# Kernel tuning notes

Measured on AMD Instinct MI355X. Metric: run time of the kernel, lower is better.

Reference implementation:

```python
import jax, jax.numpy as jnp
import numpy as np

B, LX, T = 32, 64, 128
D = 512          # d_model
DW = 512         # d_word_vec
V = 32000        # src_vocab_size
AV = 16          # trg_vocab_size (attribute vocab)
YL = 2
LSTM_IN = 2 * DW + 2 * D  # decode_on_y=True


def setup_inputs() -> dict:
    key = jax.random.key(0)
    ks = jax.random.split(key, 20)
    s = 0.02
    attr_tab = jax.random.normal(ks[10], (AV, DW), jnp.float32) * s
    attr_tab = attr_tab.at[0].set(0.0)  # padding_idx=0
    return {
        "x_enc": jax.random.normal(ks[0], (B, LX, 2 * D), jnp.float32),
        "x_enc_k": jax.random.normal(ks[1], (B, LX, D), jnp.float32),
        "dec_h0": jax.random.normal(ks[2], (B, D), jnp.float32),
        "dec_c0": jax.random.normal(ks[3], (B, D), jnp.float32),
        "x_mask": jnp.zeros((B, LX), jnp.bool_),
        "y_train": jax.random.randint(ks[4], (B, YL), 0, AV),
        "x_train": jax.random.randint(ks[5], (B, T), 0, V),
        "word_emb": jax.random.normal(ks[6], (V, DW), jnp.float32) * s,
        "attr_emb_tab": attr_tab,
        "W_ih": jax.random.normal(ks[7], (4 * D, LSTM_IN), jnp.float32) * s,
        "W_hh": jax.random.normal(ks[8], (4 * D, D), jnp.float32) * s,
        "b_ih": jnp.zeros((4 * D,), jnp.float32),
        "b_hh": jnp.zeros((4 * D,), jnp.float32),
        "W_trg": jax.random.normal(ks[9], (D, D), jnp.float32) * s,
        "b_trg": jnp.zeros((D,), jnp.float32),
        "W_att": jax.random.normal(ks[11], (1, D), jnp.float32) * s,
        "b_att": jnp.zeros((1,), jnp.float32),
        "W_cr": jax.random.normal(ks[12], (D, 3 * D), jnp.float32) * s,
        "W_ro": jax.random.normal(ks[13], (V, D), jnp.float32) * s,
    }


def _decode(x_enc, x_enc_k, dec_h0, dec_c0, y_train, x_train, word_emb,
            attr_emb_tab, W_ih, W_hh, b_ih, b_hh, W_trg, b_trg, W_att, b_att,
            W_cr, W_ro):
    x_emb = word_emb[x_train[:, :-1]]          # [B, T-1, DW]
    attr = attr_emb_tab[y_train].sum(axis=1)   # [B, DW]

    def step(carry, x_t):
        h, c, feed = carry
        inp = jnp.concatenate([x_t, attr, feed], axis=1)  # [B, 2DW+2D]
        gates = inp @ W_ih.T + b_ih + h @ W_hh.T + b_hh   # [B, 4D]
        i, f, g, o = jnp.split(gates, 4, axis=1)          # torch order i,f,g,o
        c = jax.nn.sigmoid(f) * c + jax.nn.sigmoid(i) * jnp.tanh(g)
        h = jax.nn.sigmoid(o) * jnp.tanh(c)
        # MlpAttn (attn_mask is ignored in the original)
        q = h @ W_trg.T + b_trg                            # [B, D]
        att_h = jnp.tanh(x_enc_k + q[:, None, :])          # [B, LX, D]
        scores = (att_h @ W_att.T + b_att)[..., 0]         # [B, LX]
        w = jax.nn.softmax(scores, axis=-1)
        ctx = jnp.einsum('bl,bld->bd', w, x_enc)           # [B, 2D]
        pre = jnp.tanh(jnp.concatenate([h, ctx], axis=1) @ W_cr.T)  # [B, D]
        return (h, c, ctx), pre

    feed0 = jnp.zeros((x_enc.shape[0], 2 * D), x_enc.dtype)
    xs = jnp.swapaxes(x_emb, 0, 1)                         # [T-1, B, DW]
    _, pres = jax.lax.scan(step, (dec_h0, dec_c0, feed0), xs)  # [T-1, B, D]
    logits = jnp.einsum('tbd,vd->btv', pres, W_ro)         # [B, T-1, V]
    return logits


def reference(x_enc, x_enc_k, dec_h0, dec_c0, x_mask, y_train, x_train,
              word_emb, attr_emb_tab, W_ih, W_hh, b_ih, b_hh, W_trg, b_trg,
              W_att, b_att, W_cr, W_ro):
    return _decode(x_enc, x_enc_k, dec_h0, dec_c0, y_train, x_train, word_emb,
                   attr_emb_tab, W_ih, W_hh, b_ih, b_hh, W_trg, b_trg, W_att,
                   b_att, W_cr, W_ro)
```

## Files before the change

kernel.cpp:

```cpp
#include <hip/hip_runtime.h>
#include <stdint.h>

typedef unsigned short u16;
using bf16x8 = __attribute__((ext_vector_type(8))) short;
using f32x4  = __attribute__((ext_vector_type(4))) float;

__device__ __forceinline__ float b2f(u16 v) {
  return __uint_as_float(((uint32_t)v) << 16);
}
__device__ __forceinline__ u16 f2b(float f) {
  uint32_t u = __float_as_uint(f);
  u = u + 0x7fffu + ((u >> 16) & 1u);
  return (u16)(u >> 16);
}
__device__ __forceinline__ float ldf(const void* p, size_t i, int f32) {
  return f32 ? ((const float*)p)[i] : b2f(((const u16*)p)[i]);
}
__device__ __forceinline__ float sigf(float x) {
  return __builtin_amdgcn_rcpf(1.f + __expf(-x));
}
__device__ __forceinline__ float tanhf_fast(float x) {
  x = fminf(fmaxf(x, -15.f), 15.f);
  float e = __expf(2.f * x);
  return (e - 1.f) * __builtin_amdgcn_rcpf(e + 1.f);
}

__global__ __launch_bounds__(1024) void k_detect(const u16* __restrict__ x, int* flag) {
  int tid = threadIdx.x;
  u16 v = x[tid];
  int e = (v >> 7) & 0xFF;
  int ok = (e >= 100 && e <= 140) ? 1 : 0;
#pragma unroll
  for (int o = 32; o > 0; o >>= 1) ok += __shfl_down(ok, o);
  __shared__ int s[16];
  if ((tid & 63) == 0) s[tid >> 6] = ok;
  __syncthreads();
  if (tid == 0) {
    int c = 0;
#pragma unroll
    for (int i = 0; i < 16; ++i) c += s[i];
    *flag = (c < 900) ? 1 : 0;
  }
}

__global__ __launch_bounds__(256) void k_conv(u16* __restrict__ dst, const void* __restrict__ src,
                                              int n, const int* __restrict__ flagp) {
  int f32 = *flagp;
  int i = blockIdx.x * 256 + threadIdx.x;
  if (i < n) dst[i] = f32 ? f2b(((const float*)src)[i]) : ((const u16*)src)[i];
}

__global__ __launch_bounds__(256) void k_bias(float* __restrict__ bias, const void* b_ih,
                                              const void* b_hh, const int* __restrict__ flagp) {
  int f32 = *flagp;
  int n = blockIdx.x * 256 + threadIdx.x;
  if (n < 2048) bias[n] = ldf(b_ih, n, f32) + ldf(b_hh, n, f32);
}

template<int EPI>
__global__ __launch_bounds__(256) void gemm_bt(
    const u16* __restrict__ A, int lda,
    const void* __restrict__ B, int ldb,
    int M, int K,
    void* __restrict__ C,
    const float* __restrict__ bias,
    int ldc, const int* __restrict__ flagp)
{
  __shared__ __align__(16) u16 As[128 * 32];
  __shared__ __align__(16) u16 Bs[128 * 32];
  const int f32  = *flagp;
  const int tid  = threadIdx.x;
  const int lane = tid & 63;
  const int wv   = tid >> 6;
  const int wm   = (wv >> 1) * 64;
  const int wn   = (wv & 1) * 64;
  const int n0   = blockIdx.x * 128;
  const int m0   = blockIdx.y * 128;
  const int lr   = lane & 15;
  const int lk   = (lane >> 4) * 8;

  f32x4 acc[4][4] = {};

  for (int k0 = 0; k0 < K; k0 += 32) {
    __syncthreads();
#pragma unroll
    for (int c = 0; c < 2; ++c) {
      int idx = tid + c * 256;
      int row = idx >> 2;
      int col = (idx & 3) * 8;
      int ar = m0 + row; if (ar > M - 1) ar = M - 1;
      *(uint4*)&As[idx * 8] = *(const uint4*)&A[(size_t)ar * lda + k0 + col];
      int br = n0 + row;
      if (f32) {
        const float* bp = (const float*)B + (size_t)br * ldb + k0 + col;
        float4 x0 = *(const float4*)bp;
        float4 x1 = *(const float4*)(bp + 4);
        uint4 pk;
        pk.x = (uint32_t)f2b(x0.x) | ((uint32_t)f2b(x0.y) << 16);
        pk.y = (uint32_t)f2b(x0.z) | ((uint32_t)f2b(x0.w) << 16);
        pk.z = (uint32_t)f2b(x1.x) | ((uint32_t)f2b(x1.y) << 16);
        pk.w = (uint32_t)f2b(x1.z) | ((uint32_t)f2b(x1.w) << 16);
        *(uint4*)&Bs[idx * 8] = pk;
      } else {
        *(uint4*)&Bs[idx * 8] = *(const uint4*)((const u16*)B + (size_t)br * ldb + k0 + col);
      }
    }
    __syncthreads();
    bf16x8 af[4], bfr[4];
#pragma unroll
    for (int i = 0; i < 4; ++i) {
      af[i]  = *(const bf16x8*)&As[(wm + i * 16 + lr) * 32 + lk];
      bfr[i] = *(const bf16x8*)&Bs[(wn + i * 16 + lr) * 32 + lk];
    }
#pragma unroll
    for (int i = 0; i < 4; ++i)
#pragma unroll
      for (int j = 0; j < 4; ++j)
        acc[i][j] = __builtin_amdgcn_mfma_f32_16x16x32_bf16(af[i], bfr[j], acc[i][j], 0, 0, 0);
  }

#pragma unroll
  for (int i = 0; i < 4; ++i) {
#pragma unroll
    for (int j = 0; j < 4; ++j) {
#pragma unroll
      for (int r = 0; r < 4; ++r) {
        int m = m0 + wm + i * 16 + (lane >> 4) * 4 + r;
        int n = n0 + wn + j * 16 + lr;
        if (m < M) {
          float v = acc[i][j][r];
          if (EPI == 0) {
            ((u16*)C)[(size_t)m * ldc + n] = f2b(v + bias[n]);
          } else if (EPI == 1) {
            ((u16*)C)[(size_t)m * ldc + n] = f2b(tanhf_fast(v));
          } else {
            int tt = m >> 5, bb = m & 31;
            size_t off = (size_t)bb * 4064000 + (size_t)tt * 32000 + n;
            if (f32) ((float*)C)[off] = v;
            else     ((u16*)C)[off] = f2b(v);
          }
        }
      }
    }
  }
}

__global__ __launch_bounds__(256) void k_step(
    const u16* __restrict__ inp,
    const u16* __restrict__ W3,
    const u16* __restrict__ pregates_t,
    float* __restrict__ c_state,
    u16* __restrict__ inp_next,
    u16* __restrict__ hctx_t)
{
  const int tid  = threadIdx.x;
  const int lane = tid & 63;
  const int g    = tid >> 6;
  const int c0   = blockIdx.x * 16;
  const int lr   = lane & 15;
  const int lk   = (lane >> 4) * 8;

  f32x4 acc0 = {}, acc1 = {};
  const u16* Ar = inp + lr * 1536 + lk;
  const u16* Br = W3 + (size_t)(g * 512 + c0 + lr) * 1536 + lk;
#pragma unroll 8
  for (int k0 = 0; k0 < 1536; k0 += 32) {
    bf16x8 a0 = *(const bf16x8*)(Ar + k0);
    bf16x8 a1 = *(const bf16x8*)(Ar + 16 * 1536 + k0);
    bf16x8 b  = *(const bf16x8*)(Br + k0);
    acc0 = __builtin_amdgcn_mfma_f32_16x16x32_bf16(a0, b, acc0, 0, 0, 0);
    acc1 = __builtin_amdgcn_mfma_f32_16x16x32_bf16(a1, b, acc1, 0, 0, 0);
  }

  __shared__ float gs[4][32][16];
#pragma unroll
  for (int r = 0; r < 4; ++r) {
    int mr = (lane >> 4) * 4 + r;
    gs[g][mr][lr]      = acc0[r] + b2f(pregates_t[mr * 2048 + g * 512 + c0 + lr]);
    gs[g][mr + 16][lr] = acc1[r] + b2f(pregates_t[(mr + 16) * 2048 + g * 512 + c0 + lr]);
  }
  __syncthreads();

  for (int e = tid; e < 512; e += 256) {
    int m = e >> 4, j = e & 15;
    int col = c0 + j;
    float iv = gs[0][m][j], fv = gs[1][m][j], gv = gs[2][m][j], ov = gs[3][m][j];
    float co = c_state[m * 512 + col];
    float cn = sigf(fv) * co + sigf(iv) * tanhf_fast(gv);
    float h  = sigf(ov) * tanhf_fast(cn);
    c_state[m * 512 + col] = cn;
    u16 hb = f2b(h);
    inp_next[m * 1536 + 1024 + col] = hb;
    hctx_t[m * 1536 + col] = hb;
  }
}

__global__ __launch_bounds__(512) void k_att(
    const u16* __restrict__ inp_next,
    const u16* __restrict__ x_enc_k,
    const u16* __restrict__ x_enc,
    const u16* __restrict__ W_trg,
    const u16* __restrict__ b_trg,
    const u16* __restrict__ W_att,
    const u16* __restrict__ b_att,
    u16* __restrict__ hctx_t,
    u16* __restrict__ feed_dst)
{
  const int b   = blockIdx.x;
  const int tid = threadIdx.x;
  __shared__ float hs[512], qs[512], wa[512], sc[64], wts[64];

  hs[tid] = b2f(inp_next[b * 1536 + 1024 + tid]);
  wa[tid] = b2f(W_att[tid]);
  __syncthreads();

  {
    float q = b2f(b_trg[tid]);
    const u16* wr = W_trg + tid * 512;
#pragma unroll 4
    for (int kk = 0; kk < 64; ++kk) {
      int k = kk * 8;
      bf16x8 w8 = *(const bf16x8*)(wr + k);
#pragma unroll
      for (int j = 0; j < 8; ++j)
        q += b2f((u16)w8[j]) * hs[k + j];
    }
    qs[tid] = q;
  }
  __syncthreads();

  const int wvv = tid >> 6, ln = tid & 63;
  for (int l = wvv; l < 64; l += 8) {
    float p = 0.f;
    const u16* xk = x_enc_k + ((size_t)b * 64 + l) * 512;
#pragma unroll
    for (int dd = 0; dd < 8; ++dd) {
      int d = ln + dd * 64;
      p += wa[d] * tanhf_fast(b2f(xk[d]) + qs[d]);
    }
#pragma unroll
    for (int o = 32; o > 0; o >>= 1) p += __shfl_down(p, o);
    if (ln == 0) sc[l] = p + b2f(b_att[0]);
  }
  __syncthreads();
  if (tid < 64) {
    float s = sc[tid];
    float mx = s;
#pragma unroll
    for (int o = 32; o > 0; o >>= 1) mx = fmaxf(mx, __shfl_xor(mx, o));
    float e = __expf(s - mx);
    float sm = e;
#pragma unroll
    for (int o = 32; o > 0; o >>= 1) sm += __shfl_xor(sm, o);
    wts[tid] = e * __builtin_amdgcn_rcpf(sm);
  }
  __syncthreads();
  {
    int d2 = tid * 2;
    float a0 = 0.f, a1 = 0.f;
    const u16* xe = x_enc + (size_t)b * 64 * 1024 + d2;
#pragma unroll 8
    for (int l = 0; l < 64; ++l) {
      float w = wts[l];
      uint32_t xx = *(const uint32_t*)(xe + (size_t)l * 1024);
      a0 += w * b2f((u16)(xx & 0xffffu));
      a1 += w * b2f((u16)(xx >> 16));
    }
    u16 cb0 = f2b(a0), cb1 = f2b(a1);
    feed_dst[b * 1536 + d2]     = cb0;
    feed_dst[b * 1536 + d2 + 1] = cb1;
    hctx_t[b * 1536 + 512 + d2]     = cb0;
    hctx_t[b * 1536 + 512 + d2 + 1] = cb1;
  }
}

__global__ __launch_bounds__(256) void k_gather(
    const int* __restrict__ x_train, const int* __restrict__ y_train,
    const void* __restrict__ word_emb, const void* __restrict__ attr_tab,
    u16* __restrict__ A_x, const int* __restrict__ flagp)
{
  int f32 = *flagp;
  int idx = blockIdx.x * 256 + threadIdx.x;
  if (idx >= 4064 * 1024) return;
  int m = idx >> 10, k = idx & 1023;
  int t = m >> 5, b = m & 31;
  u16 v;
  if (k < 512) {
    v = f2b(ldf(word_emb, (size_t)x_train[b * 128 + t] * 512 + k, f32));
  } else {
    int d = k - 512;
    float a = ldf(attr_tab, (size_t)y_train[b * 2] * 512 + d, f32) +
              ldf(attr_tab, (size_t)y_train[b * 2 + 1] * 512 + d, f32);
    v = f2b(a);
  }
  A_x[idx] = v;
}

__global__ __launch_bounds__(256) void k_w3(
    const void* __restrict__ W_ih, const void* __restrict__ W_hh,
    u16* __restrict__ W3, const int* __restrict__ flagp)
{
  int f32 = *flagp;
  int idx = blockIdx.x * 256 + threadIdx.x;
  if (idx >= 2048 * 1536) return;
  int n = idx / 1536, k = idx - n * 1536;
  float v = (k < 1024) ? ldf(W_ih, (size_t)n * 2048 + 1024 + k, f32)
                       : ldf(W_hh, (size_t)n * 512 + (k - 1024), f32);
  W3[idx] = f2b(v);
}

__global__ __launch_bounds__(256) void k_init(
    const void* __restrict__ dec_h0, const void* __restrict__ dec_c0,
    u16* __restrict__ inpA, float* __restrict__ c_state, const int* __restrict__ flagp)
{
  int f32 = *flagp;
  int idx = blockIdx.x * 256 + threadIdx.x;
  if (idx < 32 * 1536) {
    int m = idx / 1536, c = idx - m * 1536;
    inpA[idx] = (c < 1024) ? (u16)0 : f2b(ldf(dec_h0, m * 512 + (c - 1024), f32));
  }
  if (idx < 32 * 512) c_state[idx] = ldf(dec_c0, idx, f32);
}

extern "C" void kernel_launch(void* const* d_in, const int* in_sizes, int n_in,
                              void* d_out, int out_size, void* d_ws, size_t ws_size,
                              hipStream_t stream)
{
  const void* x_enc    = d_in[0];
  const void* x_enc_k  = d_in[1];
  const void* dec_h0   = d_in[2];
  const void* dec_c0   = d_in[3];
  const int* y_train   = (const int*)d_in[5];
  const int* x_train   = (const int*)d_in[6];
  const void* word_emb = d_in[7];
  const void* attr_tab = d_in[8];
  const void* W_ih     = d_in[9];
  const void* W_hh     = d_in[10];
  const void* b_ih     = d_in[11];
  const void* b_hh     = d_in[12];
  const void* W_trg    = d_in[13];
  const void* b_trg    = d_in[14];
  const void* W_att    = d_in[15];
  const void* b_att    = d_in[16];
  const void* W_cr     = d_in[17];
  const void* W_ro     = d_in[18];

  char* ws = (char*)d_ws;
  size_t off = 0;
  auto alloc = [&](size_t bytes) -> void* {
    void* p = ws + off;
    off += (bytes + 255) & ~(size_t)255;
    return p;
  };
  u16*   A_x      = (u16*)  alloc(4064ull * 1024 * 2);
  u16*   pregates = (u16*)  alloc(4064ull * 2048 * 2);
  u16*   W3       = (u16*)  alloc(2048ull * 1536 * 2);
  u16*   hctx     = (u16*)  alloc(4064ull * 1536 * 2);
  u16*   pre_all  = (u16*)  alloc(4064ull * 512 * 2);
  u16*   cxe      = (u16*)  alloc(32ull * 64 * 1024 * 2);
  u16*   cxek     = (u16*)  alloc(32ull * 64 * 512 * 2);
  u16*   cW_trg   = (u16*)  alloc(512ull * 512 * 2);
  u16*   cb_trg   = (u16*)  alloc(512 * 2);
  u16*   cW_att   = (u16*)  alloc(512 * 2);
  u16*   cb_att   = (u16*)  alloc(16);
  float* bias     = (float*)alloc(2048 * 4);
  u16*   inpA     = (u16*)  alloc(32 * 1536 * 2);
  u16*   inpB     = (u16*)  alloc(32 * 1536 * 2);
  float* c_state  = (float*)alloc(32 * 512 * 4);
  int*   flag     = (int*)  alloc(256);

  k_detect<<<1, 1024, 0, stream>>>((const u16*)x_enc, flag);

  k_conv<<<(2097152 + 255) / 256, 256, 0, stream>>>(cxe, x_enc, 2097152, flag);
  k_conv<<<(1048576 + 255) / 256, 256, 0, stream>>>(cxek, x_enc_k, 1048576, flag);
  k_conv<<<(262144 + 255) / 256, 256, 0, stream>>>(cW_trg, W_trg, 262144, flag);
  k_conv<<<2, 256, 0, stream>>>(cb_trg, b_trg, 512, flag);
  k_conv<<<2, 256, 0, stream>>>(cW_att, W_att, 512, flag);
  k_conv<<<1, 256, 0, stream>>>(cb_att, b_att, 1, flag);
  k_bias<<<8, 256, 0, stream>>>(bias, b_ih, b_hh, flag);

  k_init<<<192, 256, 0, stream>>>(dec_h0, dec_c0, inpA, c_state, flag);
  k_gather<<<(4064 * 1024 + 255) / 256, 256, 0, stream>>>(x_train, y_train, word_emb, attr_tab, A_x, flag);
  k_w3<<<(2048 * 1536 + 255) / 256, 256, 0, stream>>>(W_ih, W_hh, W3, flag);

  gemm_bt<0><<<dim3(16, 32), 256, 0, stream>>>(
      A_x, 1024, W_ih, 2048, 4064, 1024, pregates, bias, 2048, flag);

  for (int t = 0; t < 127; ++t) {
    const u16* cur = (t & 1) ? inpB : inpA;
    u16* nxt = (t & 1) ? inpA : inpB;
    u16* hct = hctx + (size_t)t * 32 * 1536;
    k_step<<<32, 256, 0, stream>>>(cur, W3, pregates + (size_t)t * 32 * 2048,
                                   c_state, nxt, hct);
    k_att<<<32, 512, 0, stream>>>(nxt, cxek, cxe, cW_trg, cb_trg, cW_att, cb_att,
                                  hct, nxt);
  }

  gemm_bt<1><<<dim3(4, 32), 256, 0, stream>>>(
      hctx, 1536, W_cr, 1536, 4064, 1536, pre_all, nullptr, 512, flag);
  gemm_bt<2><<<dim3(250, 32), 256, 0, stream>>>(
      pre_all, 512, W_ro, 512, 4064, 512, d_out, nullptr, 32000, flag);
}
```

Before: 6.711 ms.

## Fuse recurrent decode loop into one persistent kernel with grid barriers

Replaces the 254 per-step launches of separate LSTM-step and attention kernels with a single persistent kernel of 128 blocks that loops over all timesteps and synchronises through atomic grid barriers. Each block keeps its slice of the recurrent weights, W_trg rows, x_enc_k columns and x_enc tile resident in shared memory, which removes repeated global weight reads. The attention score is split across blocks as partial sums written to a global buffer and reduced after a barrier. The aim is to remove launch overhead and weight re-streaming, at the cost of three grid barriers per step, a dependence on all 128 blocks being co-resident, and dropping b_att (safe only because softmax is shift invariant).

```diff
diff --git a/kernel.cpp b/kernel.cpp
--- a/kernel.cpp
+++ b/kernel.cpp
@@ -145,132 +145,202 @@
   }
 }
 
-__global__ __launch_bounds__(256) void k_step(
-    const u16* __restrict__ inp,
+#define NBLK 128
+__device__ __forceinline__ void gbar(int* cnt) {
+  __syncthreads();
+  if (threadIdx.x == 0) {
+    __threadfence();
+    int t = __hip_atomic_fetch_add(cnt, 1, __ATOMIC_ACQ_REL, __HIP_MEMORY_SCOPE_AGENT);
+    int target = (t / NBLK + 1) * NBLK;
+    while (__hip_atomic_load(cnt, __ATOMIC_ACQUIRE, __HIP_MEMORY_SCOPE_AGENT) < target) {
+      __builtin_amdgcn_s_sleep(1);
+    }
+    __threadfence();
+  }
+  __syncthreads();
+}
+
+__global__ __launch_bounds__(256, 1) void k_loop(
     const u16* __restrict__ W3,
-    const u16* __restrict__ pregates_t,
-    float* __restrict__ c_state,
-    u16* __restrict__ inp_next,
-    u16* __restrict__ hctx_t)
-{
-  const int tid  = threadIdx.x;
-  const int lane = tid & 63;
-  const int g    = tid >> 6;
-  const int c0   = blockIdx.x * 16;
-  const int lr   = lane & 15;
-  const int lk   = (lane >> 4) * 8;
-
-  f32x4 acc0 = {}, acc1 = {};
-  const u16* Ar = inp + lr * 1536 + lk;
-  const u16* Br = W3 + (size_t)(g * 512 + c0 + lr) * 1536 + lk;
+    const u16* __restrict__ pregates,
+    const u16* __restrict__ cxek,
+    const u16* __restrict__ cxe,
+    const u16* __restrict__ cW_trg,
+    const u16* __restrict__ cb_trg,
+    const u16* __restrict__ cW_att,
+    const float* __restrict__ c_state,
+    u16* __restrict__ inpA,
+    u16* __restrict__ inpB,
+    u16* __restrict__ hctx,
+    float* __restrict__ ps,
+    int* __restrict__ bar)
+{
+  const int j   = blockIdx.x;
+  const int tid = threadIdx.x;
+
+  __shared__ __align__(16) u16 w3s[16][1544];
+  __shared__ __align__(16) u16 wtg[4][520];
+  __shared__ __align__(16) u16 xek[32 * 64 * 4];
+  __shared__ __align__(16) u16 xes[256 * 64];
+  __shared__ __align__(16) u16 hs[32][520];
+  __shared__ float gsum[4][32][17];
+  __shared__ float qs[128];
+  __shared__ float scp[4][64];
+  __shared__ float wts[64];
+  __shared__ float wa4[4], btg4[4];
+  __shared__ float cls[128];
+
+  for (int i = tid; i < 16 * 192; i += 256) {
+    int row = i / 192, cc = (i % 192) * 8;
+    int gr = (row >> 2) * 512 + j * 4 + (row & 3);
+    *(uint4*)&w3s[row][cc] = *(const uint4*)&W3[(size_t)gr * 1536 + cc];
+  }
+  for (int i = tid; i < 4 * 64; i += 256) {
+    int r = i >> 6, cc = (i & 63) * 8;
+    *(uint4*)&wtg[r][cc] = *(const uint4*)&cW_trg[((size_t)(j * 4 + r)) * 512 + cc];
+  }
+  for (int i = tid; i < 2048; i += 256) {
+    int b = i >> 6, l = i & 63;
+    *(uint2*)&xek[i * 4] = *(const uint2*)&cxek[((size_t)b * 64 + l) * 512 + j * 4];
+  }
+  for (int i = tid; i < 2048; i += 256) {
+    int d = i >> 3, c = i & 7;
+    bf16x8 v;
+#pragma unroll
+    for (int e = 0; e < 8; ++e)
+      v[e] = (short)cxe[((size_t)(j >> 2) * 64 + c * 8 + e) * 1024 + (j & 3) * 256 + d];
+    *(bf16x8*)&xes[d * 64 + ((c ^ (d & 7)) * 8)] = v;
+  }
+  if (tid < 4) { wa4[tid] = b2f(cW_att[j * 4 + tid]); btg4[tid] = b2f(cb_trg[j * 4 + tid]); }
+  if (tid < 128) cls[tid] = c_state[(tid >> 2) * 512 + j * 4 + (tid & 3)];
+  __syncthreads();
+
+  u16* inp  = inpA;
+  u16* inpn = inpB;
+
+  for (int t = 0; t < 127; ++t) {
+    {
+      const int lane = tid & 63, wv = tid >> 6;
+      const int lr = lane & 15, lk = (lane >> 4) * 8;
+      f32x4 acc0 = {}, acc1 = {};
+      const u16* Ar0 = inp + lr * 1536 + wv * 384 + lk;
+      const u16* Ar1 = Ar0 + 16 * 1536;
+      const u16* Br  = &w3s[lr][wv * 384 + lk];
+#pragma unroll 6
+      for (int it = 0; it < 12; ++it) {
+        bf16x8 a0 = *(const bf16x8*)(Ar0 + it * 32);
+        bf16x8 a1 = *(const bf16x8*)(Ar1 + it * 32);
+        bf16x8 bb = *(const bf16x8*)(Br + it * 32);
+        acc0 = __builtin_amdgcn_mfma_f32_16x16x32_bf16(a0, bb, acc0, 0, 0, 0);
+        acc1 = __builtin_amdgcn_mfma_f32_16x16x32_bf16(a1, bb, acc1, 0, 0, 0);
+      }
+#pragma unroll
+      for (int r = 0; r < 4; ++r) {
+        int m = (lane >> 4) * 4 + r;
+        gsum[wv][m][lr]      = acc0[r];
+        gsum[wv][m + 16][lr] = acc1[r];
+      }
+    }
+    __syncthreads();
+    if (tid < 128) {
+      const int b = tid >> 2, r = tid & 3;
+      float gv[4];
+#pragma unroll
+      for (int g = 0; g < 4; ++g) {
+        int n = g * 4 + r;
+        float s = gsum[0][b][n] + gsum[1][b][n] + gsum[2][b][n] + gsum[3][b][n];
+        gv[g] = s + b2f(pregates[((size_t)t * 32 + b) * 2048 + g * 512 + j * 4 + r]);
+      }
+      float cn = sigf(gv[1]) * cls[tid] + sigf(gv[0]) * tanhf_fast(gv[2]);
+      float hh = sigf(gv[3]) * tanhf_fast(cn);
+      cls[tid] = cn;
+      u16 hb = f2b(hh);
+      int col = j * 4 + r;
+      inpn[b * 1536 + 1024 + col] = hb;
+      hctx[((size_t)t * 32 + b) * 1536 + col] = hb;
+    }
+    gbar(bar);
+
+    for (int i = tid; i < 32 * 64; i += 256) {
+      int b = i >> 6, cc = (i & 63) * 8;
+      *(uint4*)&hs[b][cc] = *(const uint4*)&inpn[b * 1536 + 1024 + cc];
+    }
+    __syncthreads();
+    {
+      const int o = tid >> 1, kh = tid & 1;
+      const int b = o >> 2, r = o & 3;
+      float acc = 0.f;
+      const u16* hr = &hs[b][kh * 256];
+      const u16* wr = &wtg[r][kh * 256];
 #pragma unroll 8
-  for (int k0 = 0; k0 < 1536; k0 += 32) {
-    bf16x8 a0 = *(const bf16x8*)(Ar + k0);
-    bf16x8 a1 = *(const bf16x8*)(Ar + 16 * 1536 + k0);
-    bf16x8 b  = *(const bf16x8*)(Br + k0);
-    acc0 = __builtin_amdgcn_mfma_f32_16x16x32_bf16(a0, b, acc0, 0, 0, 0);
-    acc1 = __builtin_amdgcn_mfma_f32_16x16x32_bf16(a1, b, acc1, 0, 0, 0);
-  }
-
-  __shared__ float gs[4][32][16];
-#pragma unroll
-  for (int r = 0; r < 4; ++r) {
-    int mr = (lane >> 4) * 4 + r;
-    gs[g][mr][lr]      = acc0[r] + b2f(pregates_t[mr * 2048 + g * 512 + c0 + lr]);
-    gs[g][mr + 16][lr] = acc1[r] + b2f(pregates_t[(mr + 16) * 2048 + g * 512 + c0 + lr]);
-  }
-  __syncthreads();
-
-  for (int e = tid; e < 512; e += 256) {
-    int m = e >> 4, j = e & 15;
-    int col = c0 + j;
-    float iv = gs[0][m][j], fv = gs[1][m][j], gv = gs[2][m][j], ov = gs[3][m][j];
-    float co = c_state[m * 512 + col];
-    float cn = sigf(fv) * co + sigf(iv) * tanhf_fast(gv);
-    float h  = sigf(ov) * tanhf_fast(cn);
-    c_state[m * 512 + col] = cn;
-    u16 hb = f2b(h);
-    inp_next[m * 1536 + 1024 + col] = hb;
-    hctx_t[m * 1536 + col] = hb;
-  }
-}
-
-__global__ __launch_bounds__(512) void k_att(
-    const u16* __restrict__ inp_next,
-    const u16* __restrict__ x_enc_k,
-    const u16* __restrict__ x_enc,
-    const u16* __restrict__ W_trg,
-    const u16* __restrict__ b_trg,
-    const u16* __restrict__ W_att,
-    const u16* __restrict__ b_att,
-    u16* __restrict__ hctx_t,
-    u16* __restrict__ feed_dst)
-{
-  const int b   = blockIdx.x;
-  const int tid = threadIdx.x;
-  __shared__ float hs[512], qs[512], wa[512], sc[64], wts[64];
-
-  hs[tid] = b2f(inp_next[b * 1536 + 1024 + tid]);
-  wa[tid] = b2f(W_att[tid]);
-  __syncthreads();
-
-  {
-    float q = b2f(b_trg[tid]);
-    const u16* wr = W_trg + tid * 512;
-#pragma unroll 4
-    for (int kk = 0; kk < 64; ++kk) {
-      int k = kk * 8;
-      bf16x8 w8 = *(const bf16x8*)(wr + k);
-#pragma unroll
-      for (int j = 0; j < 8; ++j)
-        q += b2f((u16)w8[j]) * hs[k + j];
-    }
-    qs[tid] = q;
-  }
-  __syncthreads();
-
-  const int wvv = tid >> 6, ln = tid & 63;
-  for (int l = wvv; l < 64; l += 8) {
-    float p = 0.f;
-    const u16* xk = x_enc_k + ((size_t)b * 64 + l) * 512;
-#pragma unroll
-    for (int dd = 0; dd < 8; ++dd) {
-      int d = ln + dd * 64;
-      p += wa[d] * tanhf_fast(b2f(xk[d]) + qs[d]);
-    }
-#pragma unroll
-    for (int o = 32; o > 0; o >>= 1) p += __shfl_down(p, o);
-    if (ln == 0) sc[l] = p + b2f(b_att[0]);
-  }
-  __syncthreads();
-  if (tid < 64) {
-    float s = sc[tid];
-    float mx = s;
-#pragma unroll
-    for (int o = 32; o > 0; o >>= 1) mx = fmaxf(mx, __shfl_xor(mx, o));
-    float e = __expf(s - mx);
-    float sm = e;
-#pragma unroll
-    for (int o = 32; o > 0; o >>= 1) sm += __shfl_xor(sm, o);
-    wts[tid] = e * __builtin_amdgcn_rcpf(sm);
-  }
-  __syncthreads();
-  {
-    int d2 = tid * 2;
-    float a0 = 0.f, a1 = 0.f;
-    const u16* xe = x_enc + (size_t)b * 64 * 1024 + d2;
+      for (int k = 0; k < 256; k += 8) {
+        bf16x8 hv  = *(const bf16x8*)(hr + k);
+        bf16x8 wv8 = *(const bf16x8*)(wr + k);
+#pragma unroll
+        for (int e = 0; e < 8; ++e) acc += b2f((u16)hv[e]) * b2f((u16)wv8[e]);
+      }
+      acc += __shfl_xor(acc, 1);
+      if (kh == 0) qs[o] = acc + btg4[r];
+    }
+    __syncthreads();
+    {
+      const int b = tid >> 3, lg = tid & 7;
+      const float q0 = qs[b * 4 + 0], q1 = qs[b * 4 + 1];
+      const float q2 = qs[b * 4 + 2], q3 = qs[b * 4 + 3];
+      const float w0 = wa4[0], w1 = wa4[1], w2 = wa4[2], w3v = wa4[3];
+      float* pdst = ps + ((size_t)b * 128 + j) * 64 + lg * 8;
+#pragma unroll
+      for (int il = 0; il < 8; ++il) {
+        int l = lg * 8 + il;
+        const u16* xk = &xek[(b * 64 + l) * 4];
+        float s = w0 * tanhf_fast(b2f(xk[0]) + q0) + w1 * tanhf_fast(b2f(xk[1]) + q1)
+                + w2 * tanhf_fast(b2f(xk[2]) + q2) + w3v * tanhf_fast(b2f(xk[3]) + q3);
+        pdst[il] = s;
+      }
+    }
+    gbar(bar);
+
+    {
+      const int cb = j >> 2, dq = j & 3;
+      {
+        const int l = tid & 63, part = tid >> 6;
+        const float* pp = ps + ((size_t)cb * 128 + part * 32) * 64 + l;
+        float s = 0.f;
 #pragma unroll 8
-    for (int l = 0; l < 64; ++l) {
-      float w = wts[l];
-      uint32_t xx = *(const uint32_t*)(xe + (size_t)l * 1024);
-      a0 += w * b2f((u16)(xx & 0xffffu));
-      a1 += w * b2f((u16)(xx >> 16));
-    }
-    u16 cb0 = f2b(a0), cb1 = f2b(a1);
-    feed_dst[b * 1536 + d2]     = cb0;
-    feed_dst[b * 1536 + d2 + 1] = cb1;
-    hctx_t[b * 1536 + 512 + d2]     = cb0;
-    hctx_t[b * 1536 + 512 + d2 + 1] = cb1;
+        for (int jj = 0; jj < 32; ++jj) s += pp[jj * 64];
+        scp[part][l] = s;
+      }
+      __syncthreads();
+      if (tid < 64) {
+        float s = scp[0][tid] + scp[1][tid] + scp[2][tid] + scp[3][tid];
+        float mx = s;
+#pragma unroll
+        for (int o = 32; o > 0; o >>= 1) mx = fmaxf(mx, __shfl_xor(mx, o));
+        float e = __expf(s - mx);
+        float sm = e;
+#pragma unroll
+        for (int o = 32; o > 0; o >>= 1) sm += __shfl_xor(sm, o);
+        wts[tid] = e * __builtin_amdgcn_rcpf(sm);
+      }
+      __syncthreads();
+      {
+        float acc = 0.f;
+        const int dsw = tid & 7;
+#pragma unroll
+        for (int c = 0; c < 8; ++c) {
+          bf16x8 v = *(const bf16x8*)&xes[tid * 64 + ((c ^ dsw) * 8)];
+#pragma unroll
+          for (int e = 0; e < 8; ++e) acc += wts[c * 8 + e] * b2f((u16)v[e]);
+        }
+        u16 cv = f2b(acc);
+        int col = dq * 256 + tid;
+        inpn[cb * 1536 + col] = cv;
+        hctx[((size_t)t * 32 + cb) * 1536 + 512 + col] = cv;
+      }
+    }
+    gbar(bar);
+
+    u16* tmp = inp; inp = inpn; inpn = tmp;
   }
 }
 
@@ -311,7 +381,8 @@
 
 __global__ __launch_bounds__(256) void k_init(
     const void* __restrict__ dec_h0, const void* __restrict__ dec_c0,
-    u16* __restrict__ inpA, float* __restrict__ c_state, const int* __restrict__ flagp)
+    u16* __restrict__ inpA, float* __restrict__ c_state,
+    int* __restrict__ bar, const int* __restrict__ flagp)
 {
   int f32 = *flagp;
   int idx = blockIdx.x * 256 + threadIdx.x;
@@ -320,6 +391,7 @@
     inpA[idx] = (c < 1024) ? (u16)0 : f2b(ldf(dec_h0, m * 512 + (c - 1024), f32));
   }
   if (idx < 32 * 512) c_state[idx] = ldf(dec_c0, idx, f32);
+  if (idx < 8) bar[idx] = 0;
 }
 
 extern "C" void kernel_launch(void* const* d_in, const int* in_sizes, int n_in,
@@ -344,6 +416,7 @@
   const void* b_att    = d_in[16];
   const void* W_cr     = d_in[17];
   const void* W_ro     = d_in[18];
+  (void)b_att;
 
   char* ws = (char*)d_ws;
   size_t off = 0;
@@ -362,11 +435,12 @@
   u16*   cW_trg   = (u16*)  alloc(512ull * 512 * 2);
   u16*   cb_trg   = (u16*)  alloc(512 * 2);
   u16*   cW_att   = (u16*)  alloc(512 * 2);
-  u16*   cb_att   = (u16*)  alloc(16);
   float* bias     = (float*)alloc(2048 * 4);
   u16*   inpA     = (u16*)  alloc(32 * 1536 * 2);
   u16*   inpB     = (u16*)  alloc(32 * 1536 * 2);
   float* c_state  = (float*)alloc(32 * 512 * 4);
+  float* ps_buf   = (float*)alloc(32ull * 128 * 64 * 4);
+  int*   bar      = (int*)  alloc(256);
   int*   flag     = (int*)  alloc(256);
 
   k_detect<<<1, 1024, 0, stream>>>((const u16*)x_enc, flag);
@@ -376,25 +450,17 @@
   k_conv<<<(262144 + 255) / 256, 256, 0, stream>>>(cW_trg, W_trg, 262144, flag);
   k_conv<<<2, 256, 0, stream>>>(cb_trg, b_trg, 512, flag);
   k_conv<<<2, 256, 0, stream>>>(cW_att, W_att, 512, flag);
-  k_conv<<<1, 256, 0, stream>>>(cb_att, b_att, 1, flag);
   k_bias<<<8, 256, 0, stream>>>(bias, b_ih, b_hh, flag);
 
-  k_init<<<192, 256, 0, stream>>>(dec_h0, dec_c0, inpA, c_state, flag);
+  k_init<<<192, 256, 0, stream>>>(dec_h0, dec_c0, inpA, c_state, bar, flag);
   k_gather<<<(4064 * 1024 + 255) / 256, 256, 0, stream>>>(x_train, y_train, word_emb, attr_tab, A_x, flag);
   k_w3<<<(2048 * 1536 + 255) / 256, 256, 0, stream>>>(W_ih, W_hh, W3, flag);
 
   gemm_bt<0><<<dim3(16, 32), 256, 0, stream>>>(
       A_x, 1024, W_ih, 2048, 4064, 1024, pregates, bias, 2048, flag);
 
-  for (int t = 0; t < 127; ++t) {
-    const u16* cur = (t & 1) ? inpB : inpA;
-    u16* nxt = (t & 1) ? inpA : inpB;
-    u16* hct = hctx + (size_t)t * 32 * 1536;
-    k_step<<<32, 256, 0, stream>>>(cur, W3, pregates + (size_t)t * 32 * 2048,
-                                   c_state, nxt, hct);
-    k_att<<<32, 512, 0, stream>>>(nxt, cxek, cxe, cW_trg, cb_trg, cW_att, cb_att,
-                                  hct, nxt);
-  }
+  k_loop<<<NBLK, 256, 0, stream>>>(W3, pregates, cxek, cxe, cW_trg, cb_trg, cW_att,
+                                   c_state, inpA, inpB, hctx, ps_buf, bar);
 
   gemm_bt<1><<<dim3(4, 32), 256, 0, stream>>>(
       hctx, 1536, W_cr, 1536, 4064, 1536, pre_all, nullptr, 512, flag);
```

After: 6.549 ms. 2.4% less time.
